# Performance work log

Hardware: AMD Instinct MI355X
Metric: run time of the kernel (lower is better)

The kernel has to match this reference:

```python
import jax, jax.numpy as jnp
import numpy as np

V, E, H, L, S, T = 50257, 1024, 512, 3, 4096, 5
START, END = 3, 4  # tag_to_ix: B=0, I=1, O=2, <START>=3, <END>=4
NEG = -10000.0


def setup_inputs() -> dict:
    key = jax.random.key(0)
    ks = jax.random.split(key, 11)
    sc = 0.05
    sentence = jax.random.randint(ks[0], (S,), 0, V)
    embedding = jax.random.normal(ks[1], (V, E), jnp.float32)
    w_ih = jax.random.normal(ks[2], (L, 2, 4 * H, E), jnp.float32) * sc
    w_hh = jax.random.normal(ks[3], (L, 2, 4 * H, H), jnp.float32) * sc
    b_ih = jax.random.normal(ks[4], (L, 2, 4 * H), jnp.float32) * sc
    b_hh = jax.random.normal(ks[5], (L, 2, 4 * H), jnp.float32) * sc
    w_out = jax.random.normal(ks[6], (T, 2 * H), jnp.float32) * sc
    b_out = jax.random.normal(ks[7], (T,), jnp.float32) * sc
    transitions = jax.random.normal(ks[8], (T, T), jnp.float32)
    transitions = transitions.at[START, :].set(NEG).at[:, END].set(NEG)
    h0 = jax.random.normal(ks[9], (L, 2, H), jnp.float32)
    c0 = jax.random.normal(ks[10], (L, 2, H), jnp.float32)
    return dict(sentence=sentence, embedding=embedding, w_ih=w_ih, w_hh=w_hh,
                b_ih=b_ih, b_hh=b_hh, w_out=w_out, b_out=b_out,
                transitions=transitions, h0=h0, c0=c0)


def _lstm_dir(x, w_ih_d, w_hh_d, b_ih_d, b_hh_d, h0_d, c0_d):
    # x: [S, D_in]; one direction of one LSTM layer (PyTorch gate order i,f,g,o)
    xg = x @ w_ih_d.T + b_ih_d + b_hh_d  # [S, 4H] input projections, precomputed

    def step(carry, xg_t):
        h, c = carry
        g = xg_t + h @ w_hh_d.T
        i, f, gg, o = jnp.split(g, 4)
        i = jax.nn.sigmoid(i)
        f = jax.nn.sigmoid(f)
        gg = jnp.tanh(gg)
        o = jax.nn.sigmoid(o)
        c = f * c + i * gg
        h = o * jnp.tanh(c)
        return (h, c), h

    _, hs = jax.lax.scan(step, (h0_d, c0_d), xg)
    return hs  # [S, H]


def _bilstm_feats(sentence, embedding, w_ih, w_hh, b_ih, b_hh, w_out, b_out, h0, c0):
    x = embedding[sentence]  # [S, E]
    for l in range(L):
        fwd = _lstm_dir(x, w_ih[l, 0], w_hh[l, 0], b_ih[l, 0], b_hh[l, 0], h0[l, 0], c0[l, 0])
        bwd = _lstm_dir(x[::-1], w_ih[l, 1], w_hh[l, 1], b_ih[l, 1], b_hh[l, 1], h0[l, 1], c0[l, 1])[::-1]
        x = jnp.concatenate([fwd, bwd], axis=-1)  # [S, 2H]
    return x @ w_out.T + b_out  # [S, T] emission features


def _viterbi(feats, transitions):
    init = jnp.full((T,), NEG, feats.dtype).at[START].set(0.0)

    def step(fv, feat):
        scores = fv[None, :] + transitions  # [next_tag, prev_tag]
        bp = jnp.argmax(scores, axis=1)     # best prev tag per next tag
        return jnp.max(scores, axis=1) + feat, bp

    fv, bps = jax.lax.scan(step, init, feats)  # bps: [S, T]
    terminal = fv + transitions[END]
    best = jnp.argmax(terminal)
    path_score = terminal[best]

    def back(tag, bp):
        return bp[tag], tag

    _, rev_path = jax.lax.scan(back, best, bps[::-1])
    return path_score, rev_path[::-1]  # scalar, [S] best tag sequence


def reference(sentence, embedding, w_ih, w_hh, b_ih, b_hh, w_out, b_out, transitions, h0, c0):
    feats = _bilstm_feats(sentence, embedding, w_ih, w_hh, b_ih, b_hh, w_out, b_out, h0, c0)
    return _viterbi(feats, transitions)
```

## Files before the change

kernel.cpp:

```cpp
#include <hip/hip_runtime.h>

typedef unsigned int u32;
typedef unsigned short u16;
typedef __attribute__((ext_vector_type(4))) float f32x4;
typedef __attribute__((ext_vector_type(8))) short short8;
typedef __attribute__((ext_vector_type(4))) unsigned int u32x4;

#define S_LEN 4096
#define EDIM 1024
#define HDIM 512
#define G4 2048
#define NLAY 3
#define NTAG 5
#define NEGV -10000.0f
#define CHUNK 128
#define WARM 32
#define STEPS (WARM + CHUNK)
#define MB_SLOTS (STEPS + 1)
#define MB_U32 ((size_t)64*NLAY*MB_SLOTS*512)
#define PREP_PER_LAYER (2*G4*EDIM + 2*G4*HDIM + 4096)
#define NCH 16
#define VCL (S_LEN/NCH)
#define WARMV 64

__device__ __forceinline__ u16 tobf(float x){
  u32 u = __float_as_uint(x);
  u32 r = (u + 0x7FFFu + ((u >> 16) & 1u)) >> 16;
  return (u16)r;
}
__device__ __forceinline__ float frombf(u16 h){ return __uint_as_float(((u32)h) << 16); }
__device__ __forceinline__ float sigmf(float x){ return 1.0f / (1.0f + __expf(-x)); }
__device__ __forceinline__ float tanh_fast(float x){
  float e = __expf(-2.0f * fabsf(x));
  float t = (1.0f - e) / (1.0f + e);
  return copysignf(t, x);
}
__device__ __forceinline__ void gload_lds16(const void* g, void* l){
  __builtin_amdgcn_global_load_lds((const __attribute__((address_space(1))) u32*)g,
                                   (__attribute__((address_space(3))) u32*)l, 16, 0, 0);
}

__global__ void init_k(u32x4* mb, int n4){
  int i = blockIdx.x*256 + threadIdx.x;
  if (i < n4) mb[i] = (u32x4){0u,0u,0u,0u};
}

__global__ void gather_k(const int* __restrict__ sent, const float* __restrict__ emb, u16* __restrict__ xa){
  int idx = blockIdx.x*256 + threadIdx.x;
  int p = idx >> 8;
  int k = (idx & 255) << 2;
  int tok = sent[p];
  f32x4 v = *(const f32x4*)(emb + (size_t)tok*EDIM + k);
  u16* o = xa + (size_t)p*EDIM + k;
  o[0]=tobf(v.x); o[1]=tobf(v.y); o[2]=tobf(v.z); o[3]=tobf(v.w);
}

__global__ void prep_k(const float* __restrict__ w_ih, const float* __restrict__ w_hh,
                       const float* __restrict__ b_ih, const float* __restrict__ b_hh,
                       u16* __restrict__ wihb, u16* __restrict__ wfrag, float* __restrict__ bias){
  int gi = blockIdx.x*256 + threadIdx.x;
  if (gi >= NLAY*PREP_PER_LAYER) return;
  int lay = gi / PREP_PER_LAYER;
  int gl  = gi - lay*PREP_PER_LAYER;
  const int R0 = 2*G4*EDIM;
  const int R1 = 2*G4*HDIM;
  if (gl < R0){
    wihb[(size_t)lay*R0 + gl] = tobf(w_ih[(size_t)lay*R0 + gl]);
  } else if (gl < R0 + R1){
    int a = gl - R0;
    int e = a & 7, lane = (a>>3)&63, kk = (a>>9)&15, t = (a>>13)&15, m = (a>>17)&7, dir = (a>>20)&1;
    int row = (t>>2)*512 + m*64 + (t&3)*16 + (lane & 15);
    int k   = kk*32 + ((lane>>4)<<3) + e;
    float v = w_hh[(((size_t)lay*2 + dir)*G4 + row)*HDIM + k];
    wfrag[(size_t)lay*R1 + a] = tobf(v);
  } else {
    int b = gl - R0 - R1;
    bias[lay*4096 + b] = b_ih[(size_t)lay*2*G4 + b] + b_hh[(size_t)lay*2*G4 + b];
  }
}

__global__ __launch_bounds__(256, 1) void gemm_k(const u16* __restrict__ A, const u16* __restrict__ B,
                                                 const float* __restrict__ bias, u16* __restrict__ Cxg){
  __shared__ short aLds[2][4096];
  __shared__ short bLds[2][4096];
  int tid = threadIdx.x;
  int w = tid >> 6, l = tid & 63;
  int wr = w >> 1, wc = w & 1;
  int bx = blockIdx.x, by = blockIdx.y;
  int o0 = (0*4 + w)*1024 + l*16;
  int o1 = (1*4 + w)*1024 + l*16;
  int cb0 = o0 >> 11, r0s = (o0 >> 4) & 127;
  int cb1 = o1 >> 11, r1s = (o1 >> 4) & 127;
  const u16* a0 = A + (size_t)(by*128 + r0s)*EDIM + cb0*8;
  const u16* a1 = A + (size_t)(by*128 + r1s)*EDIM + cb1*8;
  const u16* b0 = B + (size_t)(bx*128 + r0s)*EDIM + cb0*8;
  const u16* b1 = B + (size_t)(bx*128 + r1s)*EDIM + cb1*8;

  f32x4 acc[4][4];
  #pragma unroll
  for (int i=0;i<4;i++)
    #pragma unroll
    for (int j=0;j<4;j++) acc[i][j] = (f32x4){0.f,0.f,0.f,0.f};

#define STAGE(bf_, kt_) do { \
    gload_lds16(a0 + (kt_)*32, &aLds[bf_][w*512]); \
    gload_lds16(a1 + (kt_)*32, &aLds[bf_][2048 + w*512]); \
    gload_lds16(b0 + (kt_)*32, &bLds[bf_][w*512]); \
    gload_lds16(b1 + (kt_)*32, &bLds[bf_][2048 + w*512]); \
  } while(0)

  STAGE(0, 0);
  asm volatile("s_waitcnt vmcnt(0)" ::: "memory");
  __syncthreads();
  int buf = 0;
  for (int kt = 0; kt < 32; ++kt){
    if (kt < 31){ if (buf) STAGE(0, kt+1); else STAGE(1, kt+1); }
    short8 af[4], bf[4];
    #pragma unroll
    for (int i=0;i<4;i++) af[i] = *(const short8*)&aLds[buf][(l>>4)*1024 + (wr*64 + i*16 + (l&15))*8];
    #pragma unroll
    for (int j=0;j<4;j++) bf[j] = *(const short8*)&bLds[buf][(l>>4)*1024 + (wc*64 + j*16 + (l&15))*8];
    #pragma unroll
    for (int i=0;i<4;i++)
      #pragma unroll
      for (int j=0;j<4;j++)
        acc[i][j] = __builtin_amdgcn_mfma_f32_16x16x32_bf16(af[i], bf[j], acc[i][j], 0, 0, 0);
    asm volatile("s_waitcnt vmcnt(0)" ::: "memory");
    __syncthreads();
    buf ^= 1;
  }
#undef STAGE
  #pragma unroll
  for (int j=0;j<4;j++){
    int col = bx*128 + wc*64 + j*16 + (l & 15);
    float bs = bias[col];
    #pragma unroll
    for (int i=0;i<4;i++){
      int r0 = by*128 + wr*64 + i*16 + ((l>>4)<<2);
      #pragma unroll
      for (int rr=0; rr<4; ++rr){
        float v = acc[i][j][rr] + bs;
        Cxg[(size_t)(r0+rr)*4096 + col] = tobf(v);
      }
    }
  }
}

__global__ __launch_bounds__(256, 1) void recur_k(
    int lay, const u16* __restrict__ xg, const u16* __restrict__ wfrag, u32* mbox,
    const float* __restrict__ h0, const float* __restrict__ c0, u16* __restrict__ xout)
{
  __shared__ float gldsA[256], gldsB[256];
  __shared__ alignas(16) u32 hA[256], hB[256];
  int bid = blockIdx.x;
  int xcd = bid & 7, slot = bid >> 3;
  int m = slot & 7, gg = slot >> 3;
  int gidx = xcd*4 + gg;
  int unit = gidx >> 4, g = gidx & 15;
  int cA = 2*g, cB = 2*g + 1;
  int tid = threadIdx.x, w = tid >> 6, l = tid & 63;

  u32x4 af[4][16];
  {
    const u16* wb0 = wfrag + ((size_t)((unit*8 + m)*16 + w*4))*8192 + l*8;
    #pragma unroll
    for (int j=0;j<4;j++)
      #pragma unroll
      for (int kk=0;kk<16;++kk)
        af[j][kk] = *(const u32x4*)(wb0 + (size_t)j*8192 + kk*512);
    #pragma unroll
    for (int j=0;j<4;j++)
      #pragma unroll
      for (int kk=0;kk<16;++kk)
        asm volatile("" : "+a"(af[j][kk]));
    __builtin_amdgcn_sched_barrier(0);
  }

  u32* mbA = mbox + ((size_t)((unit*32 + cA)*NLAY + lay))*MB_SLOTS*512;
  u32* mbB = mbox + ((size_t)((unit*32 + cB)*NLAY + lay))*MB_SLOTS*512;

  int base_uA = cA*CHUNK - WARM;
  int base_uB = cB*CHUNK - WARM;
  float cst = 0.f, h0f = 0.f;
  if (w == 0){ h0f = h0[unit*HDIM + m*64 + l]; cst = c0[unit*HDIM + m*64 + l]; }
  if (w == 1){ h0f = h0[unit*HDIM + m*64 + l]; cst = c0[unit*HDIM + m*64 + l]; }

#define PUBLISH(MB, SLOT, STAMP, HBI) do { \
    int b1 = __shfl((HBI), (l & ~3) + 1); \
    int b2 = __shfl((HBI), (l & ~3) + 2); \
    int b3 = __shfl((HBI), (l & ~3) + 3); \
    if ((l & 3) == 0){ \
      u32 d0 = ((u32)(HBI) & 0xffffu) | (((u32)b1 & 0xffffu) << 16); \
      u32 d1 = ((u32)b2 & 0xffffu) | (((u32)b3 & 0xffffu) << 16); \
      u32x4 val = (u32x4){(u32)(STAMP), d0, d1, 0u}; \
      u32* addr = (MB) + ((size_t)(SLOT)*512) + (m*16 + (l>>2))*4; \
      asm volatile("global_store_dwordx4 %0, %1, off sc0 sc1" :: "v"(addr), "v"(val) : "memory"); \
    } \
  } while(0)

#define POLL2LDS(MB, SLOT, STAMP, LDS) do { \
    const u32* p0 = (MB) + ((size_t)(SLOT)*512) + l*4; \
    const u32* p1 = p0 + 256; \
    u32x4 a, b; \
    int budget = 1 << 18; \
    while (true){ \
      asm volatile("global_load_dwordx4 %0, %2, off sc0 sc1\n\t" \
                   "global_load_dwordx4 %1, %3, off sc0 sc1\n\t" \
                   "s_waitcnt vmcnt(0)" \
                   : "=v"(a), "=v"(b) : "v"(p0), "v"(p1) : "memory"); \
      if (__all(a.x == (u32)(STAMP) && b.x == (u32)(STAMP))) break; \
      if (--budget <= 0) break; \
    } \
    (LDS)[2*l] = a.y; (LDS)[2*l+1] = a.z; \
    (LDS)[2*l+128] = b.y; (LDS)[2*l+129] = b.z; \
  } while(0)

  if (w == 0){ int hbi = (int)tobf(h0f); PUBLISH(mbA, 0, 1u, hbi); }
  if (w == 1){ int hbi = (int)tobf(h0f); PUBLISH(mbB, 0, 1u, hbi); }
  if (w == 2){ POLL2LDS(mbA, 0, 1u, hA); }
  if (w == 3){ POLL2LDS(mbB, 0, 1u, hB); }
  __syncthreads();

  for (int s = 0; s < STEPS; ++s){
    int u2A = base_uA + s;
    int uApos = (u2A < 0) ? 0 : u2A;
    int pA = unit ? (S_LEN-1-uApos) : uApos;
    int u2B = base_uB + s;
    int pB = unit ? (S_LEN-1-u2B) : u2B;
    float xgi=0.f, xgf=0.f, xgg=0.f, xgo=0.f;
    if (w == 0){
      const u16* xp = xg + (size_t)pA*4096 + unit*G4 + m*64 + l;
      xgi = frombf(xp[0]); xgf = frombf(xp[512]); xgg = frombf(xp[1024]); xgo = frombf(xp[1536]);
    }
    if (w == 1){
      const u16* xp = xg + (size_t)pB*4096 + unit*G4 + m*64 + l;
      xgi = frombf(xp[0]); xgf = frombf(xp[512]); xgg = frombf(xp[1024]); xgo = frombf(xp[1536]);
    }
    {
      short8 bf[16];
      #pragma unroll
      for (int kk=0; kk<16; ++kk)
        bf[kk] = __builtin_bit_cast(short8, *(const u32x4*)&hA[16*kk + 4*(l>>4)]);
      f32x4 acc[4];
      #pragma unroll
      for (int j=0;j<4;j++) acc[j] = (f32x4){0.f,0.f,0.f,0.f};
      #pragma unroll
      for (int kk=0; kk<16; ++kk)
        #pragma unroll
        for (int j=0;j<4;j++)
          asm volatile("v_mfma_f32_16x16x32_bf16 %0, %1, %2, %0"
                       : "+v"(acc[j]) : "a"(af[j][kk]), "v"(bf[kk]));
      if ((l & 15) == 0){
        #pragma unroll
        for (int j=0;j<4;j++)
          *(f32x4*)(gldsA + (w*4+j)*16 + ((l>>4)<<2)) = acc[j];
      }
    }
    {
      short8 bf[16];
      #pragma unroll
      for (int kk=0; kk<16; ++kk)
        bf[kk] = __builtin_bit_cast(short8, *(const u32x4*)&hB[16*kk + 4*(l>>4)]);
      f32x4 acc[4];
      #pragma unroll
      for (int j=0;j<4;j++) acc[j] = (f32x4){0.f,0.f,0.f,0.f};
      #pragma unroll
      for (int kk=0; kk<16; ++kk)
        #pragma unroll
        for (int j=0;j<4;j++)
          asm volatile("v_mfma_f32_16x16x32_bf16 %0, %1, %2, %0"
                       : "+v"(acc[j]) : "a"(af[j][kk]), "v"(bf[kk]));
      if ((l & 15) == 0){
        #pragma unroll
        for (int j=0;j<4;j++)
          *(f32x4*)(gldsB + (w*4+j)*16 + ((l>>4)<<2)) = acc[j];
      }
    }
    __syncthreads();
    if (w == 0){
      int sub = l >> 4, r = l & 15;
      float hv;
      if (u2A >= 0){
        float ip = gldsA[(0*4+sub)*16 + r] + xgi;
        float fp = gldsA[(1*4+sub)*16 + r] + xgf;
        float gp = gldsA[(2*4+sub)*16 + r] + xgg;
        float op = gldsA[(3*4+sub)*16 + r] + xgo;
        float ig = sigmf(ip), fg = sigmf(fp), gv = tanh_fast(gp), og = sigmf(op);
        cst = fg*cst + ig*gv;
        hv = og * tanh_fast(cst);
      } else {
        hv = h0f;
      }
      int hbi = (int)tobf(hv);
      PUBLISH(mbA, s+1, (u32)(s+2), hbi);
      if (u2A >= cA*CHUNK)
        xout[(size_t)pA*EDIM + unit*HDIM + m*64 + l] = (u16)hbi;
    }
    if (w == 1){
      int sub = l >> 4, r = l & 15;
      float ip = gldsB[(0*4+sub)*16 + r] + xgi;
      float fp = gldsB[(1*4+sub)*16 + r] + xgf;
      float gp = gldsB[(2*4+sub)*16 + r] + xgg;
      float op = gldsB[(3*4+sub)*16 + r] + xgo;
      float ig = sigmf(ip), fg = sigmf(fp), gv = tanh_fast(gp), og = sigmf(op);
      cst = fg*cst + ig*gv;
      float hv = og * tanh_fast(cst);
      int hbi = (int)tobf(hv);
      PUBLISH(mbB, s+1, (u32)(s+2), hbi);
      if (u2B >= cB*CHUNK)
        xout[(size_t)pB*EDIM + unit*HDIM + m*64 + l] = (u16)hbi;
    }
    if (w == 2 && s+1 < STEPS){ POLL2LDS(mbA, s+1, (u32)(s+2), hA); }
    if (w == 3 && s+1 < STEPS){ POLL2LDS(mbB, s+1, (u32)(s+2), hB); }
    __syncthreads();
  }
#undef PUBLISH
#undef POLL2LDS
}

__global__ void emis_k(const u16* __restrict__ x3, const float* __restrict__ wout,
                       const float* __restrict__ bout, float* __restrict__ feats){
  int w = threadIdx.x >> 6, l = threadIdx.x & 63;
  int p = blockIdx.x*16 + w;
  const short* xr = (const short*)x3 + (size_t)p*EDIM + l*16;
  short8 xv0 = *(const short8*)(xr);
  short8 xv1 = *(const short8*)(xr + 8);
  float xf[16];
  #pragma unroll
  for (int e=0;e<8;e++){ xf[e] = frombf((u16)xv0[e]); xf[8+e] = frombf((u16)xv1[e]); }
  float accv[5];
  #pragma unroll
  for (int t=0;t<5;t++){
    const float* wr = wout + t*EDIM + l*16;
    float s = 0.f;
    #pragma unroll
    for (int e=0;e<16;e++) s += xf[e]*wr[e];
    accv[t] = s;
  }
  #pragma unroll
  for (int t=0;t<5;t++){
    float s = accv[t];
    #pragma unroll
    for (int d=32; d>=1; d>>=1) s += __shfl_xor(s, d);
    if (l == 0) feats[p*NTAG + t] = s + bout[t];
  }
}

__global__ __launch_bounds__(64, 1) void vfwd_k(const float* __restrict__ feats, const float* __restrict__ trans,
                                                u32* __restrict__ bp, u32* __restrict__ bestout){
  __shared__ float fl[(VCL + WARMV)*NTAG];
  int c = blockIdx.x;
  int l = threadIdx.x;
  int t0 = c*VCL;
  int t0w = (c == 0) ? 0 : (t0 - WARMV);
  int tend = t0 + VCL;
  int nf = (tend - t0w)*NTAG;
  for (int i = l; i < nf; i += 64) fl[i] = feats[t0w*NTAG + i];
  float tr[25];
  #pragma unroll
  for (int i=0;i<25;i++) tr[i] = trans[i];
  __syncthreads();
  float fv[5];
  if (c == 0){ fv[0]=NEGV; fv[1]=NEGV; fv[2]=NEGV; fv[3]=0.0f; fv[4]=NEGV; }
  else       { fv[0]=0.f; fv[1]=0.f; fv[2]=0.f; fv[3]=0.f; fv[4]=0.f; }
  for (int t = t0w; t < tend; ++t){
    const float* ft = &fl[(t - t0w)*NTAG];
    float nfv[5];
    u32 pk = 0;
    #pragma unroll
    for (int n=0; n<5; ++n){
      float s0 = fv[0] + tr[n*5+0];
      float s1 = fv[1] + tr[n*5+1];
      float s2 = fv[2] + tr[n*5+2];
      float s3 = fv[3] + tr[n*5+3];
      float s4 = fv[4] + tr[n*5+4];
      float m = s0; u32 a = 0;
      if (s1 > m){ m = s1; a = 1; }
      if (s2 > m){ m = s2; a = 2; }
      if (s3 > m){ m = s3; a = 3; }
      if (s4 > m){ m = s4; a = 4; }
      nfv[n] = m + ft[n];
      pk |= a << (3*n);
    }
    #pragma unroll
    for (int n=0; n<5; ++n) fv[n] = nfv[n];
    if (l == 0 && t >= t0) bp[t] = pk;
  }
  if (c == NCH-1 && l == 0){
    float m = fv[0] + tr[4*5+0]; u32 a = 0;
    #pragma unroll
    for (int k=1; k<5; ++k){
      float tk = fv[k] + tr[4*5+k];
      if (tk > m){ m = tk; a = (u32)k; }
    }
    bestout[0] = a;
  }
}

__device__ __forceinline__ u32 compose_map(u32 f, u32 g){
  u32 r = 0;
  #pragma unroll
  for (int x=0;x<5;x++){
    u32 gx = (g >> (3*x)) & 7u;
    u32 fx = (f >> (3*gx)) & 7u;
    r |= fx << (3*x);
  }
  return r;
}
__global__ __launch_bounds__(1024) void vback_k(const u32* __restrict__ bp, const u32* __restrict__ best,
                                                const float* __restrict__ feats, const float* __restrict__ trans,
                                                float* __restrict__ dout){
  __shared__ u32 A[2][S_LEN];
  __shared__ u32 tg[S_LEN];
  __shared__ float red[1024];
  int tid = threadIdx.x;
  const u32 IDENT = 18056u;
  #pragma unroll
  for (int r2=0;r2<4;r2++){
    int t = tid + r2*1024;
    A[0][t] = (t < S_LEN-1) ? bp[t+1] : IDENT;
  }
  __syncthreads();
  int cur = 0;
  for (int d=1; d<S_LEN; d<<=1){
    #pragma unroll
    for (int r2=0;r2<4;r2++){
      int t = tid + r2*1024;
      u32 f = A[cur][t];
      u32 res = (t + d < S_LEN) ? compose_map(f, A[cur][t+d]) : f;
      A[cur^1][t] = res;
    }
    __syncthreads();
    cur ^= 1;
  }
  u32 b = best[0] & 7u;
  #pragma unroll
  for (int r2=0;r2<4;r2++){
    int t = tid + r2*1024;
    u32 tag = (A[cur][t] >> (3*b)) & 7u;
    dout[1 + t] = (float)tag;
    tg[t] = tag;
  }
  __syncthreads();
  float sum = 0.f;
  #pragma unroll
  for (int r2=0;r2<4;r2++){
    int t = tid + r2*1024;
    u32 tag = tg[t];
    u32 prev = (t > 0) ? tg[t-1] : 3u;
    sum += feats[t*NTAG + tag] + trans[tag*5 + prev];
  }
  red[tid] = sum;
  __syncthreads();
  for (int d2 = 512; d2 >= 1; d2 >>= 1){
    if (tid < d2) red[tid] += red[tid + d2];
    __syncthreads();
  }
  if (tid == 0) dout[0] = red[0] + trans[4*5 + tg[S_LEN-1]];
}

extern "C" void kernel_launch(void* const* d_in, const int* in_sizes, int n_in,
                              void* d_out, int out_size, void* d_ws, size_t ws_size,
                              hipStream_t stream)
{
  const int*   sent = (const int*)d_in[0];
  const float* emb  = (const float*)d_in[1];
  const float* w_ih = (const float*)d_in[2];
  const float* w_hh = (const float*)d_in[3];
  const float* b_ih = (const float*)d_in[4];
  const float* b_hh = (const float*)d_in[5];
  const float* wout = (const float*)d_in[6];
  const float* bout = (const float*)d_in[7];
  const float* trans= (const float*)d_in[8];
  const float* h0   = (const float*)d_in[9];
  const float* c0   = (const float*)d_in[10];
  float* out = (float*)d_out;
  char* ws = (char*)d_ws;
  size_t off = 0;
  auto alloc = [&](size_t bytes)->char*{
    char* pp = ws + off;
    off = (off + bytes + 255) & ~(size_t)255;
    return pp;
  };
  const size_t R0 = (size_t)2*G4*EDIM, R1 = (size_t)2*G4*HDIM;
  u16* xg     = (u16*)alloc((size_t)S_LEN*4096*2);
  u16* xa     = (u16*)alloc((size_t)S_LEN*EDIM*2);
  u16* xb     = (u16*)alloc((size_t)S_LEN*EDIM*2);
  u16* wihb   = (u16*)alloc(NLAY*R0*2);
  u16* wfrag  = (u16*)alloc(NLAY*R1*2);
  float* bias = (float*)alloc((size_t)NLAY*4096*4);
  u32* mbox   = (u32*)alloc(MB_U32*4);
  float* feats= (float*)alloc((size_t)S_LEN*NTAG*4);
  u32* bp     = (u32*)alloc((size_t)S_LEN*4);
  u32* best   = (u32*)alloc(256);
  if (off > ws_size) return;

  int n4 = (int)(MB_U32/4);
  init_k<<<(n4 + 255)/256, 256, 0, stream>>>((u32x4*)mbox, n4);
  gather_k<<<4096, 256, 0, stream>>>(sent, emb, xa);
  prep_k<<<(NLAY*PREP_PER_LAYER + 255)/256, 256, 0, stream>>>(w_ih, w_hh, b_ih, b_hh, wihb, wfrag, bias);
  u16* xin = xa; u16* xo = xb;
  for (int l2 = 0; l2 < NLAY; ++l2){
    gemm_k<<<dim3(32,32), 256, 0, stream>>>(xin, wihb + (size_t)l2*R0, bias + (size_t)l2*4096, xg);
    recur_k<<<256, 256, 0, stream>>>(l2, xg, wfrag + (size_t)l2*R1, mbox,
                                     h0 + (size_t)l2*2*HDIM, c0 + (size_t)l2*2*HDIM, xo);
    u16* tmp = xin; xin = xo; xo = tmp;
  }
  emis_k<<<256, 1024, 0, stream>>>(xin, wout, bout, feats);
  vfwd_k<<<NCH, 64, 0, stream>>>(feats, trans, bp, best);
  vback_k<<<1, 1024, 0, stream>>>(bp, best, feats, trans, out);
}
```

Before: 1.549 ms.

## Process four chunked LSTM chains per block with halved chunk length

Each recurrence block now runs four independent sequence chunks (one per wave) instead of two, and the chunk length is halved so there are 64 chains per direction. Every wave does its own gate math, mailbox publish and poll, and all four waves issue matvecs for all four chains against the shared register-resident weights. The mailbox is reused across layers through layer-offset stamps rather than separate per-layer regions. The aim is to shorten the serial step count per layer, at the cost of doubling the MFMA work per step and making the warm-up overhead a larger share of each chunk.

```diff
diff --git a/kernel.cpp b/kernel.cpp
--- a/kernel.cpp
+++ b/kernel.cpp
@@ -13,11 +13,11 @@
 #define NLAY 3
 #define NTAG 5
 #define NEGV -10000.0f
-#define CHUNK 128
+#define CHUNK 64
 #define WARM 32
 #define STEPS (WARM + CHUNK)
 #define MB_SLOTS (STEPS + 1)
-#define MB_U32 ((size_t)64*NLAY*MB_SLOTS*512)
+#define MB_U32 ((size_t)128*MB_SLOTS*512)
 #define PREP_PER_LAYER (2*G4*EDIM + 2*G4*HDIM + 4096)
 #define NCH 16
 #define VCL (S_LEN/NCH)
@@ -150,15 +150,17 @@
     int lay, const u16* __restrict__ xg, const u16* __restrict__ wfrag, u32* mbox,
     const float* __restrict__ h0, const float* __restrict__ c0, u16* __restrict__ xout)
 {
-  __shared__ float gldsA[256], gldsB[256];
-  __shared__ alignas(16) u32 hA[256], hB[256];
+  __shared__ float glds[4][256];
+  __shared__ alignas(16) u32 hL[4][256];
   int bid = blockIdx.x;
   int xcd = bid & 7, slot = bid >> 3;
   int m = slot & 7, gg = slot >> 3;
   int gidx = xcd*4 + gg;
-  int unit = gidx >> 4, g = gidx & 15;
-  int cA = 2*g, cB = 2*g + 1;
+  int unit = gidx >> 4;
+  int gbase = (gidx & 15)*4;
   int tid = threadIdx.x, w = tid >> 6, l = tid & 63;
+  int mychain = gbase + w;
+  u32 stbase = (u32)(lay*MB_SLOTS);
 
   u32x4 af[4][16];
   {
@@ -176,16 +178,13 @@
     __builtin_amdgcn_sched_barrier(0);
   }
 
-  u32* mbA = mbox + ((size_t)((unit*32 + cA)*NLAY + lay))*MB_SLOTS*512;
-  u32* mbB = mbox + ((size_t)((unit*32 + cB)*NLAY + lay))*MB_SLOTS*512;
-
-  int base_uA = cA*CHUNK - WARM;
-  int base_uB = cB*CHUNK - WARM;
-  float cst = 0.f, h0f = 0.f;
-  if (w == 0){ h0f = h0[unit*HDIM + m*64 + l]; cst = c0[unit*HDIM + m*64 + l]; }
-  if (w == 1){ h0f = h0[unit*HDIM + m*64 + l]; cst = c0[unit*HDIM + m*64 + l]; }
-
-#define PUBLISH(MB, SLOT, STAMP, HBI) do { \
+  u32* mymb = mbox + (size_t)(unit*64 + mychain)*MB_SLOTS*512;
+
+  int my_base = mychain*CHUNK - WARM;
+  float cst = c0[unit*HDIM + m*64 + l];
+  float h0f = h0[unit*HDIM + m*64 + l];
+
+#define PUBLISH(SLOT, STAMP, HBI) do { \
     int b1 = __shfl((HBI), (l & ~3) + 1); \
     int b2 = __shfl((HBI), (l & ~3) + 2); \
     int b3 = __shfl((HBI), (l & ~3) + 3); \
@@ -193,13 +192,13 @@
       u32 d0 = ((u32)(HBI) & 0xffffu) | (((u32)b1 & 0xffffu) << 16); \
       u32 d1 = ((u32)b2 & 0xffffu) | (((u32)b3 & 0xffffu) << 16); \
       u32x4 val = (u32x4){(u32)(STAMP), d0, d1, 0u}; \
-      u32* addr = (MB) + ((size_t)(SLOT)*512) + (m*16 + (l>>2))*4; \
+      u32* addr = mymb + ((size_t)(SLOT)*512) + (m*16 + (l>>2))*4; \
       asm volatile("global_store_dwordx4 %0, %1, off sc0 sc1" :: "v"(addr), "v"(val) : "memory"); \
     } \
   } while(0)
 
-#define POLL2LDS(MB, SLOT, STAMP, LDS) do { \
-    const u32* p0 = (MB) + ((size_t)(SLOT)*512) + l*4; \
+#define POLL2LDS(SLOT, STAMP) do { \
+    const u32* p0 = mymb + ((size_t)(SLOT)*512) + l*4; \
     const u32* p1 = p0 + 256; \
     u32x4 a, b; \
     int budget = 1 << 18; \
@@ -211,80 +210,58 @@
       if (__all(a.x == (u32)(STAMP) && b.x == (u32)(STAMP))) break; \
       if (--budget <= 0) break; \
     } \
-    (LDS)[2*l] = a.y; (LDS)[2*l+1] = a.z; \
-    (LDS)[2*l+128] = b.y; (LDS)[2*l+129] = b.z; \
+    hL[w][2*l] = a.y; hL[w][2*l+1] = a.z; \
+    hL[w][2*l+128] = b.y; hL[w][2*l+129] = b.z; \
   } while(0)
 
-  if (w == 0){ int hbi = (int)tobf(h0f); PUBLISH(mbA, 0, 1u, hbi); }
-  if (w == 1){ int hbi = (int)tobf(h0f); PUBLISH(mbB, 0, 1u, hbi); }
-  if (w == 2){ POLL2LDS(mbA, 0, 1u, hA); }
-  if (w == 3){ POLL2LDS(mbB, 0, 1u, hB); }
+  { int hbi = (int)tobf(h0f); PUBLISH(0, stbase + 1u, hbi); }
+  POLL2LDS(0, stbase + 1u);
   __syncthreads();
 
   for (int s = 0; s < STEPS; ++s){
-    int u2A = base_uA + s;
-    int uApos = (u2A < 0) ? 0 : u2A;
-    int pA = unit ? (S_LEN-1-uApos) : uApos;
-    int u2B = base_uB + s;
-    int pB = unit ? (S_LEN-1-u2B) : u2B;
-    float xgi=0.f, xgf=0.f, xgg=0.f, xgo=0.f;
-    if (w == 0){
-      const u16* xp = xg + (size_t)pA*4096 + unit*G4 + m*64 + l;
+    int my_u = my_base + s;
+    int my_upos = (my_u < 0) ? 0 : my_u;
+    int my_p = unit ? (S_LEN-1-my_upos) : my_upos;
+    float xgi, xgf, xgg, xgo;
+    {
+      const u16* xp = xg + (size_t)my_p*4096 + unit*G4 + m*64 + l;
       xgi = frombf(xp[0]); xgf = frombf(xp[512]); xgg = frombf(xp[1024]); xgo = frombf(xp[1536]);
     }
-    if (w == 1){
-      const u16* xp = xg + (size_t)pB*4096 + unit*G4 + m*64 + l;
-      xgi = frombf(xp[0]); xgf = frombf(xp[512]); xgg = frombf(xp[1024]); xgo = frombf(xp[1536]);
-    }
+#define CHAIN_MATVEC(ii) { \
+      short8 bf[16]; \
+      _Pragma("unroll") \
+      for (int kk=0; kk<16; ++kk) \
+        bf[kk] = __builtin_bit_cast(short8, *(const u32x4*)&hL[ii][16*kk + 4*(l>>4)]); \
+      f32x4 acc[4]; \
+      _Pragma("unroll") \
+      for (int j=0;j<4;j++) acc[j] = (f32x4){0.f,0.f,0.f,0.f}; \
+      _Pragma("unroll") \
+      for (int kk=0; kk<16; ++kk) \
+        _Pragma("unroll") \
+        for (int j=0;j<4;j++) \
+          asm volatile("v_mfma_f32_16x16x32_bf16 %0, %1, %2, %0" \
+                       : "+v"(acc[j]) : "a"(af[j][kk]), "v"(bf[kk])); \
+      if ((l & 15) == 0){ \
+        _Pragma("unroll") \
+        for (int j=0;j<4;j++) \
+          *(f32x4*)(&glds[ii][(w*4+j)*16 + ((l>>4)<<2)]) = acc[j]; \
+      } } \
+      __builtin_amdgcn_sched_barrier(0);
+    CHAIN_MATVEC(0)
+    CHAIN_MATVEC(1)
+    CHAIN_MATVEC(2)
+    CHAIN_MATVEC(3)
+#undef CHAIN_MATVEC
+    __syncthreads();
     {
-      short8 bf[16];
-      #pragma unroll
-      for (int kk=0; kk<16; ++kk)
-        bf[kk] = __builtin_bit_cast(short8, *(const u32x4*)&hA[16*kk + 4*(l>>4)]);
-      f32x4 acc[4];
-      #pragma unroll
-      for (int j=0;j<4;j++) acc[j] = (f32x4){0.f,0.f,0.f,0.f};
-      #pragma unroll
-      for (int kk=0; kk<16; ++kk)
-        #pragma unroll
-        for (int j=0;j<4;j++)
-          asm volatile("v_mfma_f32_16x16x32_bf16 %0, %1, %2, %0"
-                       : "+v"(acc[j]) : "a"(af[j][kk]), "v"(bf[kk]));
-      if ((l & 15) == 0){
-        #pragma unroll
-        for (int j=0;j<4;j++)
-          *(f32x4*)(gldsA + (w*4+j)*16 + ((l>>4)<<2)) = acc[j];
-      }
-    }
-    {
-      short8 bf[16];
-      #pragma unroll
-      for (int kk=0; kk<16; ++kk)
-        bf[kk] = __builtin_bit_cast(short8, *(const u32x4*)&hB[16*kk + 4*(l>>4)]);
-      f32x4 acc[4];
-      #pragma unroll
-      for (int j=0;j<4;j++) acc[j] = (f32x4){0.f,0.f,0.f,0.f};
-      #pragma unroll
-      for (int kk=0; kk<16; ++kk)
-        #pragma unroll
-        for (int j=0;j<4;j++)
-          asm volatile("v_mfma_f32_16x16x32_bf16 %0, %1, %2, %0"
-                       : "+v"(acc[j]) : "a"(af[j][kk]), "v"(bf[kk]));
-      if ((l & 15) == 0){
-        #pragma unroll
-        for (int j=0;j<4;j++)
-          *(f32x4*)(gldsB + (w*4+j)*16 + ((l>>4)<<2)) = acc[j];
-      }
-    }
-    __syncthreads();
-    if (w == 0){
       int sub = l >> 4, r = l & 15;
+      const float* gld = &glds[w][0];
       float hv;
-      if (u2A >= 0){
-        float ip = gldsA[(0*4+sub)*16 + r] + xgi;
-        float fp = gldsA[(1*4+sub)*16 + r] + xgf;
-        float gp = gldsA[(2*4+sub)*16 + r] + xgg;
-        float op = gldsA[(3*4+sub)*16 + r] + xgo;
+      if (my_u >= 0){
+        float ip = gld[(0*4+sub)*16 + r] + xgi;
+        float fp = gld[(1*4+sub)*16 + r] + xgf;
+        float gp = gld[(2*4+sub)*16 + r] + xgg;
+        float op = gld[(3*4+sub)*16 + r] + xgo;
         float ig = sigmf(ip), fg = sigmf(fp), gv = tanh_fast(gp), og = sigmf(op);
         cst = fg*cst + ig*gv;
         hv = og * tanh_fast(cst);
@@ -292,26 +269,11 @@
         hv = h0f;
       }
       int hbi = (int)tobf(hv);
-      PUBLISH(mbA, s+1, (u32)(s+2), hbi);
-      if (u2A >= cA*CHUNK)
-        xout[(size_t)pA*EDIM + unit*HDIM + m*64 + l] = (u16)hbi;
-    }
-    if (w == 1){
-      int sub = l >> 4, r = l & 15;
-      float ip = gldsB[(0*4+sub)*16 + r] + xgi;
-      float fp = gldsB[(1*4+sub)*16 + r] + xgf;
-      float gp = gldsB[(2*4+sub)*16 + r] + xgg;
-      float op = gldsB[(3*4+sub)*16 + r] + xgo;
-      float ig = sigmf(ip), fg = sigmf(fp), gv = tanh_fast(gp), og = sigmf(op);
-      cst = fg*cst + ig*gv;
-      float hv = og * tanh_fast(cst);
-      int hbi = (int)tobf(hv);
-      PUBLISH(mbB, s+1, (u32)(s+2), hbi);
-      if (u2B >= cB*CHUNK)
-        xout[(size_t)pB*EDIM + unit*HDIM + m*64 + l] = (u16)hbi;
-    }
-    if (w == 2 && s+1 < STEPS){ POLL2LDS(mbA, s+1, (u32)(s+2), hA); }
-    if (w == 3 && s+1 < STEPS){ POLL2LDS(mbB, s+1, (u32)(s+2), hB); }
+      PUBLISH(s+1, stbase + (u32)(s+2), hbi);
+      if (my_u >= mychain*CHUNK)
+        xout[(size_t)my_p*EDIM + unit*HDIM + m*64 + l] = (u16)hbi;
+      if (s+1 < STEPS){ POLL2LDS(s+1, stbase + (u32)(s+2)); }
+    }
     __syncthreads();
   }
 #undef PUBLISH
```

New measurement: 1.487 ms. 1.04x faster.
